# Kernel tuning notes

Measured on AMD Instinct MI355X. Metric: run time of the kernel, lower is better.

Reference implementation:

```python
import jax, jax.numpy as jnp
import numpy as np

N = 100000
E = 625000
IN_C, HID_C, OUT_C = 128, 128, 128


def setup_inputs() -> dict:
    key = jax.random.key(0)
    ks = jax.random.split(key, 8)
    x = jax.random.normal(ks[0], (N, IN_C), dtype=jnp.float32)
    edge_index = jax.random.randint(ks[1], (2, E), 0, N, dtype=jnp.int64)
    # SAGEConv layer 1: lin_l (on aggregated neighbors, with bias), lin_r (on root, no bias)
    s1 = 1.0 / np.sqrt(IN_C)
    W1l = jax.random.uniform(ks[2], (HID_C, IN_C), minval=-s1, maxval=s1, dtype=jnp.float32)
    b1l = jax.random.uniform(ks[3], (HID_C,), minval=-s1, maxval=s1, dtype=jnp.float32)
    W1r = jax.random.uniform(ks[4], (HID_C, IN_C), minval=-s1, maxval=s1, dtype=jnp.float32)
    s2 = 1.0 / np.sqrt(HID_C)
    W2l = jax.random.uniform(ks[5], (OUT_C, HID_C), minval=-s2, maxval=s2, dtype=jnp.float32)
    b2l = jax.random.uniform(ks[6], (OUT_C,), minval=-s2, maxval=s2, dtype=jnp.float32)
    W2r = jax.random.uniform(ks[7], (OUT_C, HID_C), minval=-s2, maxval=s2, dtype=jnp.float32)
    return {"x": x, "edge_index": edge_index,
            "W1l": W1l, "b1l": b1l, "W1r": W1r,
            "W2l": W2l, "b2l": b2l, "W2r": W2r}


def _sage_conv(x, src, dst, Wl, bl, Wr, num_nodes):
    # mean aggregation of source features into destination nodes
    agg = jax.ops.segment_sum(x[src], dst, num_segments=num_nodes)  # [N, d]
    cnt = jax.ops.segment_sum(jnp.ones((src.shape[0],), dtype=x.dtype), dst,
                              num_segments=num_nodes)  # [N]
    mean = agg / jnp.maximum(cnt, 1.0)[:, None]  # zero-degree nodes stay 0
    return mean @ Wl.T + bl + x @ Wr.T


def reference(x, edge_index, W1l, b1l, W1r, W2l, b2l, W2r):
    src, dst = edge_index[0], edge_index[1]
    h = jax.nn.sigmoid(_sage_conv(x, src, dst, W1l, b1l, W1r, N))
    out = _sage_conv(h, src, dst, W2l, b2l, W2r, N)
    return out
```

## Files before the change

### kernel.cpp

```cpp
#include <hip/hip_runtime.h>
#include <math.h>

#define NN 100000
#define NE 625000
#define CC 128
#define CAP 32
#define NT2 1563
#define LSTR 264

typedef __attribute__((ext_vector_type(8))) short bf16x8;
typedef __attribute__((ext_vector_type(4))) float f32x4;

__device__ __forceinline__ unsigned short f2b(float f) {
    unsigned int u = __float_as_uint(f);
    unsigned int r = (u + 0x7FFFu + ((u >> 16) & 1u)) >> 16;
    return (unsigned short)r;
}
__device__ __forceinline__ float b2f(unsigned int h) {
    return __uint_as_float(h << 16);
}


__global__ void build_kernel(const int* __restrict__ src, const int* __restrict__ dst,
                             int* __restrict__ cnt, int* __restrict__ col) {
    int e = blockIdx.x * blockDim.x + threadIdx.x;
    if (e < NE) {
        int d = dst[e];
        int p = atomicAdd(&cnt[d], 1);
        if (p < CAP) col[d * CAP + p] = src[e];
    }
}


__global__ __launch_bounds__(256) void cvtX_kernel(const float* __restrict__ x,
                                                   unsigned short* __restrict__ xb) {
    size_t i = ((size_t)blockIdx.x * 256 + threadIdx.x) * 4;
    float4 v = *(const float4*)&x[i];
    ushort2 lo = { f2b(v.x), f2b(v.y) };
    ushort2 hi = { f2b(v.z), f2b(v.w) };
    *(ushort2*)&xb[i]     = lo;
    *(ushort2*)&xb[i + 2] = hi;
}


__global__ void cvtW_kernel(const float* __restrict__ W1l, const float* __restrict__ W1r,
                            const float* __restrict__ W2l, const float* __restrict__ W2r,
                            unsigned short* __restrict__ Wcat1,
                            unsigned short* __restrict__ Wcat2) {
    int i = blockIdx.x * blockDim.x + threadIdx.x;
    int layer = i >> 15;
    int local = i & 32767;
    int c = local >> 8;
    int k = local & 255;
    const float* Wl = layer ? W2l : W1l;
    const float* Wr = layer ? W2r : W1r;
    float v = (k < CC) ? Wl[c * CC + k] : Wr[c * CC + (k - CC)];
    (layer ? Wcat2 : Wcat1)[local] = f2b(v);
}


#define ACC8(u, m) \
    s0 = fmaf(m, b2f((u).x & 0xFFFFu), s0); s1 = fmaf(m, b2f((u).x >> 16), s1); \
    s2 = fmaf(m, b2f((u).y & 0xFFFFu), s2); s3 = fmaf(m, b2f((u).y >> 16), s3); \
    s4 = fmaf(m, b2f((u).z & 0xFFFFu), s4); s5 = fmaf(m, b2f((u).z >> 16), s5); \
    s6 = fmaf(m, b2f((u).w & 0xFFFFu), s6); s7 = fmaf(m, b2f((u).w >> 16), s7);

__global__ __launch_bounds__(256) void gather_kernel(const unsigned short* __restrict__ feat,
                                                     const int* __restrict__ cnt,
                                                     const int* __restrict__ col,
                                                     unsigned short* __restrict__ aggb) {
    int gtid = blockIdx.x * blockDim.x + threadIdx.x;
    int node = gtid >> 4;
    if (node >= NN) return;
    int c8 = (gtid & 15) * 8;
    int deg = cnt[node];
    int dmin = deg < CAP ? deg : CAP;
    const int* __restrict__ bucket = col + node * CAP;
    float s0 = 0, s1 = 0, s2 = 0, s3 = 0, s4 = 0, s5 = 0, s6 = 0, s7 = 0;
    int dpad = (dmin + 7) & ~7;
    for (int j = 0; j < dpad; j += 8) {
        int   idx[8];
        float msk[8];
#pragma unroll
        for (int q = 0; q < 8; ++q) {
            int jj = j + q;
            msk[q] = jj < dmin ? 1.0f : 0.0f;
            idx[q] = jj < dmin ? jj : (dmin - 1);
        }
        uint4 u[8];
#pragma unroll
        for (int q = 0; q < 8; ++q) {
            int n = bucket[idx[q]];
            u[q] = *(const uint4*)&feat[(size_t)n * CC + c8];
        }
#pragma unroll
        for (int q = 0; q < 8; ++q) { ACC8(u[q], msk[q]); }
    }
    float iv = 1.0f / (float)(deg > 0 ? deg : 1);
    uint4 o;
    o.x = (unsigned int)f2b(s0 * iv) | ((unsigned int)f2b(s1 * iv) << 16);
    o.y = (unsigned int)f2b(s2 * iv) | ((unsigned int)f2b(s3 * iv) << 16);
    o.z = (unsigned int)f2b(s4 * iv) | ((unsigned int)f2b(s5 * iv) << 16);
    o.w = (unsigned int)f2b(s6 * iv) | ((unsigned int)f2b(s7 * iv) << 16);
    *(uint4*)&aggb[(size_t)node * CC + c8] = o;
}


template<bool SIGMOID, bool OUT_FP32>
__global__ __launch_bounds__(256, 3) void gemm3_kernel(
        const unsigned short* __restrict__ aggb,
        const unsigned short* __restrict__ featb,
        const unsigned short* __restrict__ Wcat,
        const float* __restrict__ bias,
        void* __restrict__ outv) {
    __shared__ unsigned short Acat[64 * LSTR];

    const int t    = threadIdx.x;
    const int w    = t >> 6;
    const int lane = t & 63;
    const int m    = lane & 15;
    const int kq   = lane >> 4;
    const int col0 = w * 32;

    bf16x8 breg[2][8];
#pragma unroll
    for (int ct = 0; ct < 2; ++ct)
#pragma unroll
        for (int ks = 0; ks < 8; ++ks)
            breg[ct][ks] = *(const bf16x8*)(Wcat + (size_t)(col0 + ct * 16 + m) * 256 + ks * 32 + kq * 8);

    const float bias0 = bias[col0 + m];
    const float bias1 = bias[col0 + 16 + m];

    const int sr  = t >> 2;
    const int seg = t & 3;

    for (int rt = blockIdx.x; rt < NT2; rt += gridDim.x) {
        const int row0 = rt * 64;

        int gr = row0 + sr; if (gr >= NN) gr = NN - 1;
        const unsigned short* srcp = (seg < 2)
            ? (aggb  + (size_t)gr * CC + seg * 64)
            : (featb + (size_t)gr * CC + (seg - 2) * 64);
        bf16x8 st[8];
#pragma unroll
        for (int j = 0; j < 8; ++j) st[j] = *(const bf16x8*)(srcp + j * 8);

        __syncthreads();

        unsigned short* q = &Acat[sr * LSTR + seg * 64];
#pragma unroll
        for (int j = 0; j < 8; ++j) *(bf16x8*)(q + j * 8) = st[j];

        __syncthreads();

        f32x4 acc[4][2];
#pragma unroll
        for (int rt4 = 0; rt4 < 4; ++rt4)
#pragma unroll
            for (int ct = 0; ct < 2; ++ct) acc[rt4][ct] = (f32x4)0.0f;

#pragma unroll
        for (int ks = 0; ks < 8; ++ks) {
            bf16x8 a[4];
#pragma unroll
            for (int rt4 = 0; rt4 < 4; ++rt4)
                a[rt4] = *(const bf16x8*)&Acat[(rt4 * 16 + m) * LSTR + ks * 32 + kq * 8];
#pragma unroll
            for (int rt4 = 0; rt4 < 4; ++rt4) {
                acc[rt4][0] = __builtin_amdgcn_mfma_f32_16x16x32_bf16(a[rt4], breg[0][ks], acc[rt4][0], 0, 0, 0);
                acc[rt4][1] = __builtin_amdgcn_mfma_f32_16x16x32_bf16(a[rt4], breg[1][ks], acc[rt4][1], 0, 0, 0);
            }
        }

#pragma unroll
        for (int rt4 = 0; rt4 < 4; ++rt4) {
#pragma unroll
            for (int ct = 0; ct < 2; ++ct) {
                const int c = col0 + ct * 16 + m;
                const float bv = ct ? bias1 : bias0;
#pragma unroll
                for (int i = 0; i < 4; ++i) {
                    const int r = row0 + rt4 * 16 + kq * 4 + i;
                    if (r < NN) {
                        float v = acc[rt4][ct][i] + bv;
                        if (SIGMOID) v = 1.0f / (1.0f + __expf(-v));
                        if (OUT_FP32) ((float*)outv)[(size_t)r * CC + c] = v;
                        else ((unsigned short*)outv)[(size_t)r * CC + c] = f2b(v);
                    }
                }
            }
        }
    }
}


extern "C" void kernel_launch(void* const* d_in, const int* in_sizes, int n_in,
                              void* d_out, int out_size, void* d_ws, size_t ws_size,
                              hipStream_t stream) {
    const float* x   = (const float*)d_in[0];
    const int*   ei  = (const int*)d_in[1];
    const float* W1l = (const float*)d_in[2];
    const float* b1l = (const float*)d_in[3];
    const float* W1r = (const float*)d_in[4];
    const float* W2l = (const float*)d_in[5];
    const float* b2l = (const float*)d_in[6];
    const float* W2r = (const float*)d_in[7];
    float* out = (float*)d_out;

    const int* src = ei;
    const int* dst = ei + NE;

    int* cnt = (int*)d_ws;
    int* col = cnt + NN;
    unsigned short* Wcat1 = (unsigned short*)(col + NN * CAP);
    unsigned short* Wcat2 = Wcat1 + 128 * 256;
    unsigned short* xb    = Wcat2 + 128 * 256;
    unsigned short* aggb  = xb + (size_t)NN * CC;
    unsigned short* hb    = aggb + (size_t)NN * CC;

    hipMemsetAsync(cnt, 0, (size_t)NN * sizeof(int), stream);

    build_kernel<<<(NE + 255) / 256, 256, 0, stream>>>(src, dst, cnt, col);
    cvtX_kernel<<<(NN * CC / 4) / 256, 256, 0, stream>>>(x, xb);
    cvtW_kernel<<<256, 256, 0, stream>>>(W1l, W1r, W2l, W2r, Wcat1, Wcat2);

    const int GB = 782;

    gather_kernel<<<(NN * 16) / 256, 256, 0, stream>>>(xb, cnt, col, aggb);
    gemm3_kernel<true, false><<<GB, 256, 0, stream>>>(aggb, xb, Wcat1, b1l, hb);

    gather_kernel<<<(NN * 16) / 256, 256, 0, stream>>>(hb, cnt, col, aggb);
    gemm3_kernel<false, true><<<GB, 256, 0, stream>>>(aggb, hb, Wcat2, b2l, out);
}
```

Before: 253.9 us.

## Fuse prep kernels, vectorize bucket index loads, nontemporal output stores

Merges the edge-bucket build, x conversion and weight conversion kernels into one launch, with block ranges dispatching to each task, which removes two launch gaps and lets the three tasks overlap. In the gather kernel, neighbor indices are now read as two 16-byte vector loads per 8-edge chunk instead of eight scalar loads. Padding lanes point at the chunk's first neighbor rather than the last valid one. Final fp32 output stores use nontemporal hints to avoid polluting cache; the vector bucket loads may read stale slots beyond the degree, but those are masked.

```diff
diff --git a/kernel.cpp b/kernel.cpp
--- a/kernel.cpp
+++ b/kernel.cpp
@@ -21,41 +21,44 @@
 }
 
 
-__global__ void build_kernel(const int* __restrict__ src, const int* __restrict__ dst,
-                             int* __restrict__ cnt, int* __restrict__ col) {
-    int e = blockIdx.x * blockDim.x + threadIdx.x;
-    if (e < NE) {
-        int d = dst[e];
-        int p = atomicAdd(&cnt[d], 1);
-        if (p < CAP) col[d * CAP + p] = src[e];
+#define PREP_BUILD_B 2442
+#define PREP_CVTX_B  12500
+#define PREP_TOTAL_B (PREP_BUILD_B + PREP_CVTX_B + 256)
+
+__global__ __launch_bounds__(256) void prep_kernel(
+        const int* __restrict__ src, const int* __restrict__ dst,
+        int* __restrict__ cnt, int* __restrict__ col,
+        const float* __restrict__ x, unsigned short* __restrict__ xb,
+        const float* __restrict__ W1l, const float* __restrict__ W1r,
+        const float* __restrict__ W2l, const float* __restrict__ W2r,
+        unsigned short* __restrict__ Wcat1, unsigned short* __restrict__ Wcat2) {
+    const int bid = blockIdx.x;
+    const int tid = threadIdx.x;
+    if (bid < PREP_BUILD_B) {
+        int e = bid * 256 + tid;
+        if (e < NE) {
+            int d = dst[e];
+            int p = atomicAdd(&cnt[d], 1);
+            if (p < CAP) col[d * CAP + p] = src[e];
+        }
+    } else if (bid < PREP_BUILD_B + PREP_CVTX_B) {
+        size_t i = ((size_t)(bid - PREP_BUILD_B) * 256 + tid) * 4;
+        float4 v = *(const float4*)&x[i];
+        ushort2 lo = { f2b(v.x), f2b(v.y) };
+        ushort2 hi = { f2b(v.z), f2b(v.w) };
+        *(ushort2*)&xb[i]     = lo;
+        *(ushort2*)&xb[i + 2] = hi;
+    } else {
+        int i = (bid - PREP_BUILD_B - PREP_CVTX_B) * 256 + tid;
+        int layer = i >> 15;
+        int local = i & 32767;
+        int c = local >> 8;
+        int k = local & 255;
+        const float* Wl = layer ? W2l : W1l;
+        const float* Wr = layer ? W2r : W1r;
+        float v = (k < CC) ? Wl[c * CC + k] : Wr[c * CC + (k - CC)];
+        (layer ? Wcat2 : Wcat1)[local] = f2b(v);
     }
-}
-
-
-__global__ __launch_bounds__(256) void cvtX_kernel(const float* __restrict__ x,
-                                                   unsigned short* __restrict__ xb) {
-    size_t i = ((size_t)blockIdx.x * 256 + threadIdx.x) * 4;
-    float4 v = *(const float4*)&x[i];
-    ushort2 lo = { f2b(v.x), f2b(v.y) };
-    ushort2 hi = { f2b(v.z), f2b(v.w) };
-    *(ushort2*)&xb[i]     = lo;
-    *(ushort2*)&xb[i + 2] = hi;
-}
-
-
-__global__ void cvtW_kernel(const float* __restrict__ W1l, const float* __restrict__ W1r,
-                            const float* __restrict__ W2l, const float* __restrict__ W2r,
-                            unsigned short* __restrict__ Wcat1,
-                            unsigned short* __restrict__ Wcat2) {
-    int i = blockIdx.x * blockDim.x + threadIdx.x;
-    int layer = i >> 15;
-    int local = i & 32767;
-    int c = local >> 8;
-    int k = local & 255;
-    const float* Wl = layer ? W2l : W1l;
-    const float* Wr = layer ? W2r : W1r;
-    float v = (k < CC) ? Wl[c * CC + k] : Wr[c * CC + (k - CC)];
-    (layer ? Wcat2 : Wcat1)[local] = f2b(v);
 }
 
 
@@ -79,20 +82,24 @@
     float s0 = 0, s1 = 0, s2 = 0, s3 = 0, s4 = 0, s5 = 0, s6 = 0, s7 = 0;
     int dpad = (dmin + 7) & ~7;
     for (int j = 0; j < dpad; j += 8) {
-        int   idx[8];
+        uint4 bA = *(const uint4*)&bucket[j];
+        uint4 bB = *(const uint4*)&bucket[j + 4];
+        int nfb = (int)bA.x;
+        int nb[8] = { (int)bA.x, (int)bA.y, (int)bA.z, (int)bA.w,
+                      (int)bB.x, (int)bB.y, (int)bB.z, (int)bB.w };
+        int   n[8];
         float msk[8];
+        int rem = dmin - j;
 #pragma unroll
         for (int q = 0; q < 8; ++q) {
-            int jj = j + q;
-            msk[q] = jj < dmin ? 1.0f : 0.0f;
-            idx[q] = jj < dmin ? jj : (dmin - 1);
+            bool valid = q < rem;
+            msk[q] = valid ? 1.0f : 0.0f;
+            n[q]   = valid ? nb[q] : nfb;
         }
         uint4 u[8];
 #pragma unroll
-        for (int q = 0; q < 8; ++q) {
-            int n = bucket[idx[q]];
-            u[q] = *(const uint4*)&feat[(size_t)n * CC + c8];
-        }
+        for (int q = 0; q < 8; ++q)
+            u[q] = *(const uint4*)&feat[(size_t)n[q] * CC + c8];
 #pragma unroll
         for (int q = 0; q < 8; ++q) { ACC8(u[q], msk[q]); }
     }
@@ -185,7 +192,7 @@
                     if (r < NN) {
                         float v = acc[rt4][ct][i] + bv;
                         if (SIGMOID) v = 1.0f / (1.0f + __expf(-v));
-                        if (OUT_FP32) ((float*)outv)[(size_t)r * CC + c] = v;
+                        if (OUT_FP32) __builtin_nontemporal_store(v, &((float*)outv)[(size_t)r * CC + c]);
                         else ((unsigned short*)outv)[(size_t)r * CC + c] = f2b(v);
                     }
                 }
@@ -221,9 +228,8 @@
 
     hipMemsetAsync(cnt, 0, (size_t)NN * sizeof(int), stream);
 
-    build_kernel<<<(NE + 255) / 256, 256, 0, stream>>>(src, dst, cnt, col);
-    cvtX_kernel<<<(NN * CC / 4) / 256, 256, 0, stream>>>(x, xb);
-    cvtW_kernel<<<256, 256, 0, stream>>>(W1l, W1r, W2l, W2r, Wcat1, Wcat2);
+    prep_kernel<<<PREP_TOTAL_B, 256, 0, stream>>>(src, dst, cnt, col, x, xb,
+                                                  W1l, W1r, W2l, W2r, Wcat1, Wcat2);
 
     const int GB = 782;
 
```

Result: no change. 253.0 us (median of 2 runs) (-0.3%).
